# Kernel tuning notes

Hardware: AMD Instinct MI355X
Metric: run time of the kernel (lower is better)

Reference implementation:

```python
import jax, jax.numpy as jnp
import numpy as np

HIDDEN, NQ, NKV, HD, INTER = 2048, 8, 1, 256, 8192
B, S = 4, 2048
EPS = 1e-6
ROPE_BASE = 10000.0


def ada_rms(x, t, w, tw):
    # x: (b,s,h), t: (b,h). RMS-normalize, then modulate gain with time embedding:
    # out = normed * w * (1 + t @ tw.T)
    n = x * jax.lax.rsqrt(jnp.mean(jnp.square(x), axis=-1, keepdims=True) + EPS)
    scale = t @ tw.T  # (b,h)
    return n * (w * (1.0 + scale))[:, None, :]


def apply_rope(x, pos_ids):
    # x: (b,nh,s,hd), pos_ids: (b,s)
    half = HD // 2
    inv_freq = 1.0 / (ROPE_BASE ** (jnp.arange(0, HD, 2, dtype=jnp.float32) / HD))  # (hd/2,)
    ang = pos_ids.astype(jnp.float32)[:, :, None] * inv_freq  # (b,s,hd/2)
    cos = jnp.concatenate([jnp.cos(ang), jnp.cos(ang)], axis=-1)[:, None]  # (b,1,s,hd)
    sin = jnp.concatenate([jnp.sin(ang), jnp.sin(ang)], axis=-1)[:, None]
    x1, x2 = x[..., :half], x[..., half:]
    rot = jnp.concatenate([-x2, x1], axis=-1)
    return x * cos + rot * sin


def setup_inputs() -> dict:
    key = jax.random.key(0)
    ks = jax.random.split(key, 12)
    f32 = jnp.float32
    inp = {
        "x": jax.random.normal(ks[0], (B, S, HIDDEN), f32),
        "pos_ids": jnp.broadcast_to(jnp.arange(S, dtype=jnp.int32), (B, S)),
        "time_emb": jax.random.normal(ks[1], (B, HIDDEN), f32),
        "ln1_w": jnp.ones((HIDDEN,), f32),
        "ln1_tw": jax.random.normal(ks[2], (HIDDEN, HIDDEN), f32) * 0.02,
        "ln2_w": jnp.ones((HIDDEN,), f32),
        "ln2_tw": jax.random.normal(ks[3], (HIDDEN, HIDDEN), f32) * 0.02,
        "Wq": jax.random.normal(ks[4], (NQ * HD, HIDDEN), f32) * 0.02,
        "Wk": jax.random.normal(ks[5], (NKV * HD, HIDDEN), f32) * 0.02,
        "Wv": jax.random.normal(ks[6], (NKV * HD, HIDDEN), f32) * 0.02,
        "Wo": jax.random.normal(ks[7], (HIDDEN, NQ * HD), f32) * 0.02,
        "Wg": jax.random.normal(ks[8], (INTER, HIDDEN), f32) * 0.02,
        "Wu": jax.random.normal(ks[9], (INTER, HIDDEN), f32) * 0.02,
        "Wd": jax.random.normal(ks[10], (HIDDEN, INTER), f32) * 0.02,
    }
    return inp


def reference(x, pos_ids, time_emb, ln1_w, ln1_tw, ln2_w, ln2_tw,
              Wq, Wk, Wv, Wo, Wg, Wu, Wd):
    b, s, _ = x.shape
    g = NQ // NKV  # kv groups
    res = x
    h = ada_rms(x, time_emb, ln1_w, ln1_tw)
    q = (h @ Wq.T).reshape(b, s, NQ, HD).transpose(0, 2, 1, 3)   # (b,nq,s,hd)
    k = (h @ Wk.T).reshape(b, s, NKV, HD).transpose(0, 2, 1, 3)  # (b,nkv,s,hd)
    v = (h @ Wv.T).reshape(b, s, NKV, HD).transpose(0, 2, 1, 3)
    q = apply_rope(q, pos_ids)
    k = apply_rope(k, pos_ids)
    # GQA: group query heads over shared kv heads without materializing expanded k/v
    qg = q.reshape(b, NKV, g, s, HD)
    scores = jnp.einsum("bkgsd,bktd->bkgst", qg, k) / jnp.sqrt(jnp.float32(HD))
    attn = jax.nn.softmax(scores, axis=-1)  # (b,nkv,g,s,s) — full, no causal mask
    ctx = jnp.einsum("bkgst,bktd->bkgsd", attn, v)
    ctx = ctx.reshape(b, NQ, s, HD).transpose(0, 2, 1, 3).reshape(b, s, NQ * HD)
    x = res + ctx @ Wo.T
    res = x
    h = ada_rms(x, time_emb, ln2_w, ln2_tw)
    mlp = (jax.nn.silu(h @ Wg.T) * (h @ Wu.T)) @ Wd.T
    return res + mlp
```

## Files before the change

### kernel.cpp

```cpp
#include <hip/hip_runtime.h>

typedef unsigned short u16;
typedef unsigned int   u32;
typedef __bf16  bf16x8 __attribute__((ext_vector_type(8)));
typedef float   f32x4  __attribute__((ext_vector_type(4)));
typedef u16     u16x4  __attribute__((ext_vector_type(4)));
typedef u16     u16x8  __attribute__((ext_vector_type(8)));

#define HID 2048
#define SEQ 2048
#define BB  4
#define NQH 8
#define HD_ 256
#define INTER_ 8192

__device__ __forceinline__ float b2f(u16 u) {
  union { float f; u32 i; } x; x.i = ((u32)u) << 16; return x.f;
}
__device__ __forceinline__ u16 f2b(float f) {
  u32 u = __float_as_uint(f);
  u32 r = u + 0x7fffu + ((u >> 16) & 1u);
  return (u16)(r >> 16);
}
__device__ __forceinline__ float wsum(float v) {
#pragma unroll
  for (int m = 1; m < 64; m <<= 1) v += __shfl_xor(v, m, 64);
  return v;
}
__device__ __forceinline__ float wmax(float v) {
#pragma unroll
  for (int m = 1; m < 64; m <<= 1) v = fmaxf(v, __shfl_xor(v, m, 64));
  return v;
}
__device__ __forceinline__ void gload_lds16(const void* gp, void* lp) {
  __builtin_amdgcn_global_load_lds(
      (const __attribute__((address_space(1))) void*)gp,
      (__attribute__((address_space(3))) void*)lp, 16, 0, 0);
}
__device__ __forceinline__ void xcd_swizzle(int& bx, int& by) {
  const int nx = gridDim.x, ny = gridDim.y;
  const int nwg = nx * ny;
  if ((nwg & 7) == 0) {
    const int orig = by * nx + bx;
    const int q = nwg >> 3;
    const int wg = (orig & 7) * q + (orig >> 3);
    bx = wg % nx; by = wg / nx;
  }
}

__global__ __launch_bounds__(256) void cvt_kernel(const float* __restrict__ src,
                                                  u16* __restrict__ dst, int n4) {
  int i = blockIdx.x * 256 + threadIdx.x;
  if (i < n4) {
    const float4 v = *(const float4*)(src + (size_t)i * 4);
    u16x4 o;
    o[0] = f2b(v.x); o[1] = f2b(v.y); o[2] = f2b(v.z); o[3] = f2b(v.w);
    *(u16x4*)(dst + (size_t)i * 4) = o;
  }
}

__global__ __launch_bounds__(256) void scale_kernel(
    const float* __restrict__ temb,
    const float* __restrict__ w1, const float* __restrict__ tw1,
    const float* __restrict__ w2, const float* __restrict__ tw2,
    float* __restrict__ sf1, float* __restrict__ sf2) {
  const int wave = threadIdx.x >> 6, lane = threadIdx.x & 63;
  const int o = blockIdx.x * 4 + wave;
  const int set = o / (BB * HID);
  const int r = o % (BB * HID);
  const int b = r / HID, n = r % HID;
  const float* tw = set ? tw2 : tw1;
  const float* w  = set ? w2  : w1;
  float* sf       = set ? sf2 : sf1;
  const float* tv  = temb + (size_t)b * HID;
  const float* twr = tw + (size_t)n * HID;
  float acc = 0.f;
#pragma unroll
  for (int q = 0; q < 8; ++q) {
    const float4 a = *(const float4*)(tv + q * 256 + lane * 4);
    const float4 c = *(const float4*)(twr + q * 256 + lane * 4);
    acc += a.x * c.x + a.y * c.y + a.z * c.z + a.w * c.w;
  }
  acc = wsum(acc);
  if (lane == 0) sf[(size_t)b * HID + n] = w[n] * (1.0f + acc);
}

__global__ __launch_bounds__(256) void rope_table_kernel(const int* __restrict__ pos_ids,
                                                         float* __restrict__ cosT,
                                                         float* __restrict__ sinT) {
  const int idx = blockIdx.x * 256 + threadIdx.x;
  const int j = idx & 127, bs = idx >> 7;
  const float pos = (float)pos_ids[bs];
  const float inv = exp2f(-(float)j * (13.287712379549449f / 128.0f));
  const float ang = pos * inv;
  float sv, cv;
  sincosf(ang, &sv, &cv);
  cosT[idx] = cv; sinT[idx] = sv;
}

__global__ __launch_bounds__(256) void rmsnorm_kernel(const float* __restrict__ xin,
                                                      const float* __restrict__ sfac,
                                                      u16* __restrict__ out) {
  const int row = blockIdx.x;
  const int b = row >> 11;
  const float* xr = xin + (size_t)row * HID + threadIdx.x * 8;
  const float4 v0 = *(const float4*)(xr);
  const float4 v1 = *(const float4*)(xr + 4);
  float v[8] = {v0.x, v0.y, v0.z, v0.w, v1.x, v1.y, v1.z, v1.w};
  float ss = 0.f;
#pragma unroll
  for (int j = 0; j < 8; ++j) ss += v[j] * v[j];
  ss = wsum(ss);
  __shared__ float red[4];
  const int wave = threadIdx.x >> 6, lane = threadIdx.x & 63;
  if (lane == 0) red[wave] = ss;
  __syncthreads();
  const float tot = red[0] + red[1] + red[2] + red[3];
  const float rs = rsqrtf(tot * (1.0f / HID) + 1e-6f);
  const float* sf = sfac + (size_t)b * HID + threadIdx.x * 8;
  u16* op = out + (size_t)row * HID + threadIdx.x * 8;
  u16x8 o;
#pragma unroll
  for (int j = 0; j < 8; ++j) o[j] = f2b(v[j] * rs * sf[j]);
  *(u16x8*)op = o;
}

template <int EPI>
__global__ __launch_bounds__(256) void gemm_bt(const u16* __restrict__ A,
                                               const u16* __restrict__ B,
                                               const float* __restrict__ Res,
                                               void* __restrict__ Cv,
                                               int K, int lda, int ldb, int ldc,
                                               size_t aZ, size_t cZ) {
  A += blockIdx.z * aZ;
  __shared__ u16 As[2][128 * 32];
  __shared__ u16 Bs[2][128 * 32];
  int bx = blockIdx.x, by = blockIdx.y;
  xcd_swizzle(bx, by);
  const int m0 = bx * 128, n0 = by * 128;
  const int wave = threadIdx.x >> 6, lane = threadIdx.x & 63;
  const int wr = wave >> 1, wc = wave & 1;
  const int l15 = lane & 15, l4 = lane >> 4;

  auto stage = [&](int buf, int kt) {
#pragma unroll
    for (int j = 0; j < 2; ++j) {
      const int c = threadIdx.x + j * 256;
      const int row = c >> 2, col8 = (c & 3) << 3;
      gload_lds16(A + (size_t)(m0 + row) * lda + kt + col8, &As[buf][c * 8]);
      gload_lds16(B + (size_t)(n0 + row) * ldb + kt + col8, &Bs[buf][c * 8]);
    }
  };

  f32x4 acc[4][4] = {};

  stage(0, 0);
  int cur = 0;
  for (int kt = 0; kt < K; kt += 32) {
    __syncthreads();
    if (kt + 32 < K) stage(cur ^ 1, kt + 32);
    bf16x8 af[4], bf[4];
#pragma unroll
    for (int ms = 0; ms < 4; ++ms)
      af[ms] = *(const bf16x8*)(&As[cur][(wr * 64 + ms * 16 + l15) * 32 + l4 * 8]);
#pragma unroll
    for (int ns = 0; ns < 4; ++ns)
      bf[ns] = *(const bf16x8*)(&Bs[cur][(wc * 64 + ns * 16 + l15) * 32 + l4 * 8]);
#pragma unroll
    for (int ms = 0; ms < 4; ++ms)
#pragma unroll
      for (int ns = 0; ns < 4; ++ns)
        acc[ms][ns] = __builtin_amdgcn_mfma_f32_16x16x32_bf16(af[ms], bf[ns], acc[ms][ns], 0, 0, 0);
    cur ^= 1;
  }

  u16* Cb = (u16*)Cv + blockIdx.z * cZ;
  float* Cf = (float*)Cv + blockIdx.z * cZ;
#pragma unroll
  for (int ms = 0; ms < 4; ++ms)
#pragma unroll
    for (int i = 0; i < 4; ++i) {
      const int row = m0 + wr * 64 + ms * 16 + l4 * 4 + i;
#pragma unroll
      for (int ns = 0; ns < 4; ++ns) {
        const int col = n0 + wc * 64 + ns * 16 + l15;
        const size_t idx = (size_t)row * ldc + col;
        const float v = acc[ms][ns][i];
        if constexpr (EPI == 0) {
          Cb[idx] = f2b(v);
        } else if constexpr (EPI == 1) {
          const float g = b2f(Cb[idx]);
          Cb[idx] = f2b(g / (1.0f + __expf(-g)) * v);
        } else if constexpr (EPI == 2) {
          Cf[idx] = v + Res[idx];
        } else {
          Cf[idx] = v + Cf[idx];
        }
      }
    }
}

__global__ __launch_bounds__(256) void rope_apply_kernel(u16* __restrict__ qkv,
                                                         const float* __restrict__ cosT,
                                                         const float* __restrict__ sinT,
                                                         u16* __restrict__ vt) {
  const int tok = blockIdx.x;
  const int b = tok >> 11, s = tok & 2047;
  u16* rowp = qkv + (size_t)tok * 2560;
  const float* ct = cosT + (size_t)tok * 128;
  const float* st = sinT + (size_t)tok * 128;
  for (int p = threadIdx.x; p < 1024; p += 256) {
    const int h = p >> 7, j = p & 127;
    u16* e = rowp + h * 256 + j;
    const float x1 = b2f(e[0]), x2 = b2f(e[128]);
    const float c = ct[j], sn = st[j];
    e[0]   = f2b((x1 * c - x2 * sn) * 0.0625f);
    e[128] = f2b((x2 * c + x1 * sn) * 0.0625f);
  }
  if (threadIdx.x < 128) {
    const int j = threadIdx.x;
    u16* e = rowp + 2048 + j;
    const float x1 = b2f(e[0]), x2 = b2f(e[128]);
    const float c = ct[j], sn = st[j];
    e[0]   = f2b(x1 * c - x2 * sn);
    e[128] = f2b(x2 * c + x1 * sn);
  }
  {
    const int d = threadIdx.x;
    vt[((size_t)b * HD_ + d) * SEQ + s] = rowp[2304 + d];
  }
}

__global__ __launch_bounds__(256) void softmax_kernel(u16* __restrict__ Sb) {
  const int row = blockIdx.x;
  u16* rp = Sb + (size_t)row * 2048 + threadIdx.x * 8;
  const u16x8 t = *(const u16x8*)rp;
  float v[8];
#pragma unroll
  for (int j = 0; j < 8; ++j) v[j] = b2f(t[j]);
  float m = v[0];
#pragma unroll
  for (int j = 1; j < 8; ++j) m = fmaxf(m, v[j]);
  m = wmax(m);
  __shared__ float redm[4], reds[4];
  const int wave = threadIdx.x >> 6, lane = threadIdx.x & 63;
  if (lane == 0) redm[wave] = m;
  __syncthreads();
  m = fmaxf(fmaxf(redm[0], redm[1]), fmaxf(redm[2], redm[3]));
  float s = 0.f;
#pragma unroll
  for (int j = 0; j < 8; ++j) { v[j] = __expf(v[j] - m); s += v[j]; }
  s = wsum(s);
  if (lane == 0) reds[wave] = s;
  __syncthreads();
  const float inv = 1.0f / (reds[0] + reds[1] + reds[2] + reds[3]);
  u16x8 o;
#pragma unroll
  for (int j = 0; j < 8; ++j) o[j] = f2b(v[j] * inv);
  *(u16x8*)rp = o;
}

extern "C" void kernel_launch(void* const* d_in, const int* in_sizes, int n_in,
                              void* d_out, int out_size, void* d_ws, size_t ws_size,
                              hipStream_t stream) {
  const float* x     = (const float*)d_in[0];
  const int*   pos   = (const int*)d_in[1];
  const float* temb  = (const float*)d_in[2];
  const float* ln1w  = (const float*)d_in[3];
  const float* ln1tw = (const float*)d_in[4];
  const float* ln2w  = (const float*)d_in[5];
  const float* ln2tw = (const float*)d_in[6];
  const float* Wq    = (const float*)d_in[7];
  const float* Wk    = (const float*)d_in[8];
  const float* Wv    = (const float*)d_in[9];
  const float* Wo    = (const float*)d_in[10];
  const float* Wg    = (const float*)d_in[11];
  const float* Wu    = (const float*)d_in[12];
  const float* Wd    = (const float*)d_in[13];
  float* out = (float*)d_out;

  char* ws = (char*)d_ws;
  constexpr size_t OFF_SF1  = 0;
  constexpr size_t OFF_SF2  = 32768;
  constexpr size_t OFF_COS  = 65536;
  constexpr size_t OFF_SIN  = 4259840;
  constexpr size_t OFF_WQKV = 8454144;
  constexpr size_t OFF_WO   = 18939904;
  constexpr size_t OFF_WG   = 27328512;
  constexpr size_t OFF_WU   = 60882944;
  constexpr size_t OFF_WD   = 94437376;
  constexpr size_t OFF_H    = 127991808;
  constexpr size_t OFF_QKV  = 161546240;
  constexpr size_t OFF_VT   = 203489280;
  constexpr size_t OFF_CTX  = 207683584;
  constexpr size_t REQUIRED = 241238016;

  float* sf1 = (float*)(ws + OFF_SF1);
  float* sf2 = (float*)(ws + OFF_SF2);
  float* cosT = (float*)(ws + OFF_COS);
  float* sinT = (float*)(ws + OFF_SIN);
  u16* wqkv = (u16*)(ws + OFF_WQKV);
  u16* wo   = (u16*)(ws + OFF_WO);
  u16* wg   = (u16*)(ws + OFF_WG);
  u16* wu   = (u16*)(ws + OFF_WU);
  u16* wd   = (u16*)(ws + OFF_WD);
  u16* hbuf = (u16*)(ws + OFF_H);
  u16* qkv  = (u16*)(ws + OFF_QKV);
  u16* vt   = (u16*)(ws + OFF_VT);
  u16* ctx  = (u16*)(ws + OFF_CTX);
  u16* inter = (u16*)(ws + OFF_QKV);
  u16* Sbuf = (u16*)d_out;

  if (ws_size < REQUIRED) return;

  auto cvt = [&](const float* s, u16* d, size_t n) {
    int n4 = (int)(n / 4);
    cvt_kernel<<<(n4 + 255) / 256, 256, 0, stream>>>(s, d, n4);
  };

  cvt(Wq, wqkv,                      (size_t)2048 * HID);
  cvt(Wk, wqkv + (size_t)2048 * HID, (size_t)256 * HID);
  cvt(Wv, wqkv + (size_t)2304 * HID, (size_t)256 * HID);
  cvt(Wo, wo, (size_t)HID * HID);
  cvt(Wg, wg, (size_t)INTER_ * HID);
  cvt(Wu, wu, (size_t)INTER_ * HID);
  cvt(Wd, wd, (size_t)HID * INTER_);

  scale_kernel<<<(2 * BB * HID) / 4, 256, 0, stream>>>(temb, ln1w, ln1tw, ln2w, ln2tw, sf1, sf2);
  rope_table_kernel<<<(BB * SEQ * 128) / 256, 256, 0, stream>>>(pos, cosT, sinT);

  rmsnorm_kernel<<<BB * SEQ, 256, 0, stream>>>(x, sf1, hbuf);

  gemm_bt<0><<<dim3(64, 20), 256, 0, stream>>>(hbuf, wqkv, nullptr, qkv, HID, HID, HID, 2560, 0, 0);

  rope_apply_kernel<<<BB * SEQ, 256, 0, stream>>>(qkv, cosT, sinT, vt);

  for (int b = 0; b < BB; ++b) {
    const u16* qb = qkv + (size_t)b * SEQ * 2560;
    const u16* kb = qb + 2048;
    const u16* vb = vt + (size_t)b * HD_ * SEQ;
    u16* cb = ctx + (size_t)b * SEQ * HID;
    gemm_bt<0><<<dim3(16, 16, 8), 256, 0, stream>>>(
        qb, kb, nullptr, Sbuf, HD_, 2560, 2560, SEQ, (size_t)HD_, (size_t)SEQ * SEQ);
    softmax_kernel<<<NQH * SEQ, 256, 0, stream>>>(Sbuf);
    gemm_bt<0><<<dim3(16, 2, 8), 256, 0, stream>>>(
        Sbuf, vb, nullptr, cb, SEQ, SEQ, SEQ, HID, (size_t)SEQ * SEQ, (size_t)HD_);
  }

  gemm_bt<2><<<dim3(64, 16), 256, 0, stream>>>(ctx, wo, x, out, HID, HID, HID, HID, 0, 0);

  rmsnorm_kernel<<<BB * SEQ, 256, 0, stream>>>(out, sf2, hbuf);

  constexpr int MC = BB * SEQ / 2;
  for (int c = 0; c < 2; ++c) {
    const u16* hA = hbuf + (size_t)c * MC * HID;
    float* outC = out + (size_t)c * MC * HID;
    gemm_bt<0><<<dim3(MC / 128, INTER_ / 128), 256, 0, stream>>>(hA, wg, nullptr, inter, HID, HID, HID, INTER_, 0, 0);
    gemm_bt<1><<<dim3(MC / 128, INTER_ / 128), 256, 0, stream>>>(hA, wu, nullptr, inter, HID, HID, HID, INTER_, 0, 0);
    gemm_bt<3><<<dim3(MC / 128, HID / 128),    256, 0, stream>>>(inter, wd, nullptr, outC, INTER_, INTER_, INTER_, HID, 0, 0);
  }

  (void)in_sizes; (void)n_in; (void)out_size;
}
```

Baseline: 1.965 ms.

## Triple-buffer GEMM LDS staging with XOR swizzle and vmcnt-based waits

Moves the bf16 GEMM from double to triple buffering, prefetching two K-tiles ahead. The full __syncthreads is replaced by an explicit vmcnt wait plus s_barrier, so loads for the next tiles can stay in flight while the current tile is computed. The global-to-LDS column chunks are also XOR-swizzled by row to cut LDS bank conflicts on the fragment reads. Costs 50% more LDS per block, which may lower occupancy, and depends on the hand-counted vmcnt(4) being correct.

```diff
diff --git a/kernel.cpp b/kernel.cpp
--- a/kernel.cpp
+++ b/kernel.cpp
@@ -133,8 +133,8 @@
                                                int K, int lda, int ldb, int ldc,
                                                size_t aZ, size_t cZ) {
   A += blockIdx.z * aZ;
-  __shared__ u16 As[2][128 * 32];
-  __shared__ u16 Bs[2][128 * 32];
+  __shared__ u16 As[3][128 * 32];
+  __shared__ u16 Bs[3][128 * 32];
   int bx = blockIdx.x, by = blockIdx.y;
   xcd_swizzle(bx, by);
   const int m0 = bx * 128, n0 = by * 128;
@@ -142,36 +142,51 @@
   const int wr = wave >> 1, wc = wave & 1;
   const int l15 = lane & 15, l4 = lane >> 4;
 
+  const int c0 = threadIdx.x,        r0 = c0 >> 2, u0 = c0 & 3;
+  const int c1 = threadIdx.x + 256,  r1 = c1 >> 2, u1 = c1 & 3;
+  const int s0 = (u0 ^ ((r0 >> 1) & 3)) << 3;
+  const int s1 = (u1 ^ ((r1 >> 1) & 3)) << 3;
+
   auto stage = [&](int buf, int kt) {
-#pragma unroll
-    for (int j = 0; j < 2; ++j) {
-      const int c = threadIdx.x + j * 256;
-      const int row = c >> 2, col8 = (c & 3) << 3;
-      gload_lds16(A + (size_t)(m0 + row) * lda + kt + col8, &As[buf][c * 8]);
-      gload_lds16(B + (size_t)(n0 + row) * ldb + kt + col8, &Bs[buf][c * 8]);
-    }
+    gload_lds16(A + (size_t)(m0 + r0) * lda + kt + s0, &As[buf][c0 * 8]);
+    gload_lds16(B + (size_t)(n0 + r0) * ldb + kt + s0, &Bs[buf][c0 * 8]);
+    gload_lds16(A + (size_t)(m0 + r1) * lda + kt + s1, &As[buf][c1 * 8]);
+    gload_lds16(B + (size_t)(n0 + r1) * ldb + kt + s1, &Bs[buf][c1 * 8]);
   };
 
   f32x4 acc[4][4] = {};
 
   stage(0, 0);
+  stage(1, 32);
   int cur = 0;
   for (int kt = 0; kt < K; kt += 32) {
-    __syncthreads();
-    if (kt + 32 < K) stage(cur ^ 1, kt + 32);
+    if (kt + 32 < K) {
+      asm volatile("s_waitcnt vmcnt(4)" ::: "memory");
+    } else {
+      asm volatile("s_waitcnt vmcnt(0)" ::: "memory");
+    }
+    __builtin_amdgcn_s_barrier();
+    if (kt + 64 < K) {
+      const int nxt = (cur == 0) ? 2 : cur - 1;
+      stage(nxt, kt + 64);
+    }
     bf16x8 af[4], bf[4];
 #pragma unroll
-    for (int ms = 0; ms < 4; ++ms)
-      af[ms] = *(const bf16x8*)(&As[cur][(wr * 64 + ms * 16 + l15) * 32 + l4 * 8]);
-#pragma unroll
-    for (int ns = 0; ns < 4; ++ns)
-      bf[ns] = *(const bf16x8*)(&Bs[cur][(wc * 64 + ns * 16 + l15) * 32 + l4 * 8]);
+    for (int ms = 0; ms < 4; ++ms) {
+      const int r = wr * 64 + ms * 16 + l15;
+      af[ms] = *(const bf16x8*)(&As[cur][r * 32 + ((l4 ^ ((r >> 1) & 3)) << 3)]);
+    }
+#pragma unroll
+    for (int ns = 0; ns < 4; ++ns) {
+      const int r = wc * 64 + ns * 16 + l15;
+      bf[ns] = *(const bf16x8*)(&Bs[cur][r * 32 + ((l4 ^ ((r >> 1) & 3)) << 3)]);
+    }
 #pragma unroll
     for (int ms = 0; ms < 4; ++ms)
 #pragma unroll
       for (int ns = 0; ns < 4; ++ns)
         acc[ms][ns] = __builtin_amdgcn_mfma_f32_16x16x32_bf16(af[ms], bf[ns], acc[ms][ns], 0, 0, 0);
-    cur ^= 1;
+    cur = (cur == 2) ? 0 : cur + 1;
   }
 
   u16* Cb = (u16*)Cv + blockIdx.z * cZ;
```

New measurement: 1.976 ms. About the same (+0.6%).
